# Performance work log

Hardware: AMD Instinct MI355X
Metric: run time of the kernel (lower is better)

## Reference

```python
import jax, jax.numpy as jnp
import numpy as np

N = 100000      # nodes
E = 1_600_000   # edges
IN = 128        # in_channels
HID = 32        # hidden_channels (per head)
HEADS = 4
NC = 10         # num_classes
NEG_SLOPE = 0.2 # GATConv leaky relu slope
BN_EPS = 1e-5


def _gat_conv(x, src, dst, W, a_src, a_dst, bias, heads, out_ch, concat):
    # x: [N, F_in]; W: [F_in, heads*out_ch]; a_src/a_dst: [heads, out_ch]
    n = x.shape[0]
    h = (x @ W).reshape(n, heads, out_ch)                    # [N,H,C]
    al_src = jnp.sum(h * a_src, axis=-1)                     # [N,H]
    al_dst = jnp.sum(h * a_dst, axis=-1)                     # [N,H]
    e = jax.nn.leaky_relu(al_src[src] + al_dst[dst], NEG_SLOPE)  # [E,H]
    # segment softmax over destination node
    m = jax.ops.segment_max(e, dst, num_segments=n)          # [N,H]
    ex = jnp.exp(e - m[dst])
    s = jax.ops.segment_sum(ex, dst, num_segments=n)         # [N,H]
    alpha = ex / (s[dst] + 1e-16)                            # [E,H]
    out = jax.ops.segment_sum(h[src] * alpha[:, :, None], dst, num_segments=n)  # [N,H,C]
    if concat:
        out = out.reshape(n, heads * out_ch)
    else:
        out = out.mean(axis=1)
    return out + bias


def _bn(x, gamma, beta, mean, var):
    # eval-mode BatchNorm1d with running stats
    return (x - mean) * jax.lax.rsqrt(var + BN_EPS) * gamma + beta


def setup_inputs() -> dict:
    key = jax.random.key(0)
    ks = iter(jax.random.split(key, 40))
    d = {}
    d['x'] = jax.random.normal(next(ks), (N, IN), dtype=jnp.float32)
    d['edge_index'] = jax.random.randint(next(ks), (2, E), 0, N, dtype=jnp.int32)
    dims = [(IN, HID, HEADS), (HID * HEADS, HID, HEADS), (HID * HEADS, HID, 1)]
    for i, (fin, c, h) in enumerate(dims):
        d[f'W{i}'] = jax.random.normal(next(ks), (fin, h * c), dtype=jnp.float32) * (1.0 / np.sqrt(fin))
        d[f'as{i}'] = jax.random.normal(next(ks), (h, c), dtype=jnp.float32) * 0.1
        d[f'ad{i}'] = jax.random.normal(next(ks), (h, c), dtype=jnp.float32) * 0.1
        bdim = h * c if i < 2 else c
        d[f'b{i}'] = jnp.zeros((bdim,), dtype=jnp.float32)
        d[f'g{i}'] = jax.random.uniform(next(ks), (bdim,), dtype=jnp.float32, minval=0.5, maxval=1.5)
        d[f'bt{i}'] = jax.random.normal(next(ks), (bdim,), dtype=jnp.float32) * 0.1
        d[f'm{i}'] = jax.random.normal(next(ks), (bdim,), dtype=jnp.float32) * 0.1
        d[f'v{i}'] = jax.random.uniform(next(ks), (bdim,), dtype=jnp.float32, minval=0.5, maxval=1.5)
    d['Wc'] = jax.random.normal(next(ks), (HID, NC), dtype=jnp.float32) * (1.0 / np.sqrt(HID))
    d['bc'] = jnp.zeros((NC,), dtype=jnp.float32)
    return d


def reference(x, edge_index, W0, as0, ad0, b0, g0, bt0, m0, v0,
              W1, as1, ad1, b1, g1, bt1, m1, v1,
              W2, as2, ad2, b2, g2, bt2, m2, v2, Wc, bc):
    src, dst = edge_index[0], edge_index[1]
    # layer 0: concat heads
    h = _gat_conv(x, src, dst, W0, as0, ad0, b0, HEADS, HID, True)
    h = jax.nn.elu(_bn(h, g0, bt0, m0, v0))
    # layer 1: concat heads
    h = _gat_conv(h, src, dst, W1, as1, ad1, b1, HEADS, HID, True)
    h = jax.nn.elu(_bn(h, g1, bt1, m1, v1))
    # layer 2: single head, no concat
    h = _gat_conv(h, src, dst, W2, as2, ad2, b2, 1, HID, False)
    h = jax.nn.elu(_bn(h, g2, bt2, m2, v2))
    # dropout is identity in eval mode
    return h @ Wc + bc
```

## Files before the change

kernel.cpp:

```cpp
#include <hip/hip_runtime.h>
#include <hip/hip_bf16.h>
#include <math.h>

#define NN   100000
#define NE   1600000
#define FIN  128
#define HID  32
#define NHEADS 4
#define NCLS 10

typedef unsigned int uint32;
typedef __fp16 half2_t __attribute__((ext_vector_type(2)));
typedef __fp16 half8_t __attribute__((ext_vector_type(8)));
typedef float  f32x4   __attribute__((ext_vector_type(4)));

__device__ __forceinline__ uint32 packh2(float a, float b) {
    half2_t h = __builtin_amdgcn_cvt_pkrtz(a, b);
    return __builtin_bit_cast(uint32, h);
}
__device__ __forceinline__ float h_lo(uint32 v) {
    return (float)__builtin_bit_cast(half2_t, v)[0];
}
__device__ __forceinline__ float h_hi(uint32 v) {
    return (float)__builtin_bit_cast(half2_t, v)[1];
}
__device__ __forceinline__ half8_t as_h8(uint4 v) {
    return __builtin_bit_cast(half8_t, v);
}

__global__ void zero_i32(int* __restrict__ p, int n) {
    int i = blockIdx.x * blockDim.x + threadIdx.x;
    if (i < n) p[i] = 0;
}

__global__ void hist_rank_kernel(const int* __restrict__ dst, int* __restrict__ cnt,
                                 int* __restrict__ rank, int e) {
    const int t0 = blockIdx.x * (blockDim.x * 4) + threadIdx.x;
    int d[4];
    bool a[4];
#pragma unroll
    for (int k = 0; k < 4; ++k) {
        const int j = t0 + k * 256;
        a[k] = (j < e);
        d[k] = a[k] ? dst[j] : 0;
    }
    int r[4];
#pragma unroll
    for (int k = 0; k < 4; ++k)
        if (a[k]) r[k] = atomicAdd(&cnt[d[k]], 1);
#pragma unroll
    for (int k = 0; k < 4; ++k) {
        const int j = t0 + k * 256;
        if (a[k]) rank[j] = r[k];
    }
}

__global__ void scan_block_sums(const int* __restrict__ cnt, int* __restrict__ bsum, int n) {
    __shared__ int sm[256];
    int i = blockIdx.x * 256 + threadIdx.x;
    int v = (i < n) ? cnt[i] : 0;
    sm[threadIdx.x] = v;
    __syncthreads();
    for (int off = 128; off > 0; off >>= 1) {
        if (threadIdx.x < off) sm[threadIdx.x] += sm[threadIdx.x + off];
        __syncthreads();
    }
    if (threadIdx.x == 0) bsum[blockIdx.x] = sm[0];
}

__global__ void scan_single(const int* __restrict__ bsum, int* __restrict__ boff, int nb) {
    __shared__ int sm[512];
    int t = threadIdx.x;
    int v = (t < nb) ? bsum[t] : 0;
    sm[t] = v;
    __syncthreads();
    for (int off = 1; off < 512; off <<= 1) {
        int u = (t >= off) ? sm[t - off] : 0;
        __syncthreads();
        sm[t] += u;
        __syncthreads();
    }
    if (t < nb) boff[t] = sm[t] - v;
}

__global__ void scan_final(const int* __restrict__ cnt, const int* __restrict__ boff,
                           int* __restrict__ rowptr, int n) {
    __shared__ int sm[256];
    int i = blockIdx.x * 256 + threadIdx.x;
    int v = (i < n) ? cnt[i] : 0;
    sm[threadIdx.x] = v;
    __syncthreads();
    for (int off = 1; off < 256; off <<= 1) {
        int u = (threadIdx.x >= off) ? sm[threadIdx.x - off] : 0;
        __syncthreads();
        sm[threadIdx.x] += u;
        __syncthreads();
    }
    int incl = sm[threadIdx.x];
    int excl = incl - v;
    if (i < n) rowptr[i] = boff[blockIdx.x] + excl;
    if (i == n - 1) rowptr[n] = boff[blockIdx.x] + incl;
}

__global__ void scatter_kernel(const int* __restrict__ src, const int* __restrict__ dst,
                               const int* __restrict__ rank, const int* __restrict__ rowptr,
                               int* __restrict__ esrc, int e) {
    const int t0 = blockIdx.x * (blockDim.x * 4) + threadIdx.x;
#pragma unroll
    for (int k = 0; k < 4; ++k) {
        const int j = t0 + k * 256;
        if (j < e) {
            const int d = dst[j];
            esrc[rowptr[d] + rank[j]] = src[j];
        }
    }
}

__global__ void conv_x_kernel(const float* __restrict__ x, uint32* __restrict__ Xh, int n4) {
    int i = blockIdx.x * blockDim.x + threadIdx.x;
    if (i >= n4) return;
    const float4 v = ((const float4*)x)[i];
    ((uint2*)Xh)[i] = make_uint2(packh2(v.x, v.y), packh2(v.z, v.w));
}

__global__ void conv_w_kernel(const float* __restrict__ W0, const float* __restrict__ W1,
                              const float* __restrict__ W2, uint32* __restrict__ Wt0,
                              uint32* __restrict__ Wt1, uint32* __restrict__ Wt2) {
    int t = blockIdx.x * blockDim.x + threadIdx.x;
    if (t < 8192) {
        const int nn = t >> 6, ku = t & 63;
        Wt0[t] = packh2(W0[(2 * ku) * 128 + nn], W0[(2 * ku + 1) * 128 + nn]);
    } else if (t < 16384) {
        const int l = t - 8192;
        const int nn = l >> 6, ku = l & 63;
        Wt1[l] = packh2(W1[(2 * ku) * 128 + nn], W1[(2 * ku + 1) * 128 + nn]);
    } else if (t < 18432) {
        const int l = t - 16384;
        const int nn = l >> 6, ku = l & 63;
        Wt2[l] = packh2(W2[(2 * ku) * 32 + nn], W2[(2 * ku + 1) * 32 + nn]);
    }
}

__global__ void bn_prep_kernel(
    const float* __restrict__ b0, const float* __restrict__ g0, const float* __restrict__ bt0,
    const float* __restrict__ m0, const float* __restrict__ v0,
    const float* __restrict__ b1, const float* __restrict__ g1, const float* __restrict__ bt1,
    const float* __restrict__ m1, const float* __restrict__ v1,
    const float* __restrict__ b2, const float* __restrict__ g2, const float* __restrict__ bt2,
    const float* __restrict__ m2, const float* __restrict__ v2,
    float* __restrict__ A, float* __restrict__ B) {
    const int t = threadIdx.x;
    const float *b, *g, *bt, *m, *v;
    int c;
    if (t < 128)      { b = b0; g = g0; bt = bt0; m = m0; v = v0; c = t; }
    else if (t < 256) { b = b1; g = g1; bt = bt1; m = m1; v = v1; c = t - 128; }
    else if (t < 288) { b = b2; g = g2; bt = bt2; m = m2; v = v2; c = t - 256; }
    else return;
    const float s = g[c] * rsqrtf(v[c] + 1e-5f);
    A[t] = s;
    B[t] = bt[c] + (b[c] - m[c]) * s;
}

template <int FOUT, int H>
__global__ __launch_bounds__(256) void gemm_mfma(const uint32* __restrict__ Xh,
                                                 const uint32* __restrict__ Wt,
                                                 const float* __restrict__ a_s,
                                                 const float* __restrict__ a_d,
                                                 float* __restrict__ alS,
                                                 float* __restrict__ alD,
                                                 uint32* __restrict__ Outh, int n) {
    constexpr int NT = FOUT / 16;
    const int wave = threadIdx.x >> 6;
    const int lane = threadIdx.x & 63;
    const int c = lane & 15;
    const int q = lane >> 4;
    const int row0 = blockIdx.x * 128 + wave * 32;

    int r0 = row0 + c;
    int r1 = row0 + 16 + c;
    if (r0 >= n) r0 = n - 1;
    if (r1 >= n) r1 = n - 1;

    f32x4 acc[2][NT];
#pragma unroll
    for (int m = 0; m < 2; ++m)
#pragma unroll
        for (int nt = 0; nt < NT; ++nt) acc[m][nt] = (f32x4){0.f, 0.f, 0.f, 0.f};

    const uint4* XU = (const uint4*)Xh;
    const uint4* WU = (const uint4*)Wt;

#pragma unroll
    for (int ks = 0; ks < 4; ++ks) {
        const half8_t a0 = as_h8(XU[(size_t)r0 * 16 + ks * 4 + q]);
        const half8_t a1 = as_h8(XU[(size_t)r1 * 16 + ks * 4 + q]);
#pragma unroll
        for (int nt = 0; nt < NT; ++nt) {
            const half8_t b = as_h8(WU[(nt * 16 + c) * 16 + ks * 4 + q]);
            acc[0][nt] = __builtin_amdgcn_mfma_f32_16x16x32_f16(a0, b, acc[0][nt], 0, 0, 0);
            acc[1][nt] = __builtin_amdgcn_mfma_f32_16x16x32_f16(a1, b, acc[1][nt], 0, 0, 0);
        }
    }

    float asv[NT], adv[NT];
#pragma unroll
    for (int nt = 0; nt < NT; ++nt) {
        asv[nt] = a_s[c + 16 * nt];
        adv[nt] = a_d[c + 16 * nt];
    }

#pragma unroll
    for (int m = 0; m < 2; ++m) {
#pragma unroll
        for (int reg = 0; reg < 4; ++reg) {
            const int grow = row0 + m * 16 + q * 4 + reg;
            const bool ok = (grow < n);
            if constexpr (H == 4) {
                float ps[4], pd[4];
#pragma unroll
                for (int h = 0; h < 4; ++h) {
                    ps[h] = acc[m][2 * h][reg] * asv[2 * h] + acc[m][2 * h + 1][reg] * asv[2 * h + 1];
                    pd[h] = acc[m][2 * h][reg] * adv[2 * h] + acc[m][2 * h + 1][reg] * adv[2 * h + 1];
                }
#pragma unroll
                for (int off = 1; off < 16; off <<= 1) {
#pragma unroll
                    for (int h = 0; h < 4; ++h) {
                        ps[h] += __shfl_xor(ps[h], off);
                        pd[h] += __shfl_xor(pd[h], off);
                    }
                }
                if (c < 4 && ok) {
                    const float vs = (c == 0) ? ps[0] : (c == 1) ? ps[1] : (c == 2) ? ps[2] : ps[3];
                    const float vd = (c == 0) ? pd[0] : (c == 1) ? pd[1] : (c == 2) ? pd[2] : pd[3];
                    alS[(size_t)grow * 4 + c] = vs;
                    alD[(size_t)grow * 4 + c] = vd;
                }
            } else {
                float ps = acc[m][0][reg] * asv[0] + acc[m][1][reg] * asv[1];
                float pd = acc[m][0][reg] * adv[0] + acc[m][1][reg] * adv[1];
#pragma unroll
                for (int off = 1; off < 16; off <<= 1) {
                    ps += __shfl_xor(ps, off);
                    pd += __shfl_xor(pd, off);
                }
                if (c == 0 && ok) {
                    alS[grow] = ps;
                    alD[grow] = pd;
                }
            }
#pragma unroll
            for (int nt = 0; nt < NT; ++nt) {
                const float v = acc[m][nt][reg];
                const float o = __shfl_xor(v, 1);
                if (((c & 1) == 0) && ok) {
                    Outh[(size_t)grow * (FOUT / 2) + nt * 8 + (c >> 1)] = packh2(v, o);
                }
            }
        }
    }
}

template <int H, int C>
__global__ __launch_bounds__(256) void gat_aggregate(
    const uint32* __restrict__ Hb,
    const int* __restrict__ rowptr, const int* __restrict__ esrc,
    const float* __restrict__ alS, const float* __restrict__ alD,
    const float* __restrict__ bnA, const float* __restrict__ bnB,
    uint32* __restrict__ B16, int n) {
    constexpr int F    = H * C;
    constexpr int RU4  = F / 8;
    constexpr int SLOTS = 64 / RU4;
    constexpr int UNROLL = 16 / SLOTS;

    const int wave = threadIdx.x >> 6;
    const int lane = threadIdx.x & 63;
    int d = blockIdx.x * 4 + wave;
    if (d >= n) return;
    d = __builtin_amdgcn_readfirstlane(d);

    const int li = lane & (RU4 - 1);
    const int g  = lane / RU4;
    const int head = (H == 4) ? (li >> 2) : 0;

    const float ald = alD[(size_t)d * H + head];
    const int beg = rowptr[d];
    const int end = rowptr[d + 1];
    const int endm1 = end - 1;

    float acc[8];
#pragma unroll
    for (int k = 0; k < 8; ++k) acc[k] = 0.f;
    float den = 0.f;

    const uint4* HbU4 = (const uint4*)Hb;

    for (int base = beg; base < end; base += 16) {
#pragma unroll
        for (int u = 0; u < UNROLL; ++u) {
            const int j  = base + u * SLOTS + g;
            const bool act = (j < end);
            const int jc = act ? j : endm1;
            const int sj = esrc[jc];
            const float aw = (H == 4) ? alS[(size_t)sj * 4 + head] : alS[sj];
            float t = aw + ald;
            t = fmaxf(t, 0.2f * t);
            const float ex = act ? __expf(t) : 0.f;
            den += ex;
            const uint4 v = HbU4[(size_t)sj * RU4 + li];
            acc[0] = fmaf(h_lo(v.x), ex, acc[0]);
            acc[1] = fmaf(h_hi(v.x), ex, acc[1]);
            acc[2] = fmaf(h_lo(v.y), ex, acc[2]);
            acc[3] = fmaf(h_hi(v.y), ex, acc[3]);
            acc[4] = fmaf(h_lo(v.z), ex, acc[4]);
            acc[5] = fmaf(h_hi(v.z), ex, acc[5]);
            acc[6] = fmaf(h_lo(v.w), ex, acc[6]);
            acc[7] = fmaf(h_hi(v.w), ex, acc[7]);
        }
    }

#pragma unroll
    for (int off = RU4; off < 64; off <<= 1) {
#pragma unroll
        for (int k = 0; k < 8; ++k) acc[k] += __shfl_xor(acc[k], off);
        den += __shfl_xor(den, off);
    }

    if (lane < RU4) {
        const float inv = 1.f / (den + 1e-16f);
        const int c0 = 8 * li;
        const float4 A0 = *(const float4*)(bnA + c0);
        const float4 A1 = *(const float4*)(bnA + c0 + 4);
        const float4 B0 = *(const float4*)(bnB + c0);
        const float4 B1 = *(const float4*)(bnB + c0 + 4);
        const float As[8] = {A0.x, A0.y, A0.z, A0.w, A1.x, A1.y, A1.z, A1.w};
        const float Bs[8] = {B0.x, B0.y, B0.z, B0.w, B1.x, B1.y, B1.z, B1.w};
        float y[8];
#pragma unroll
        for (int k = 0; k < 8; ++k) {
            const float yy = acc[k] * inv * As[k] + Bs[k];
            y[k] = yy > 0.f ? yy : expm1f(yy);
        }
        uint4 o;
        o.x = packh2(y[0], y[1]);
        o.y = packh2(y[2], y[3]);
        o.z = packh2(y[4], y[5]);
        o.w = packh2(y[6], y[7]);
        ((uint4*)B16)[(size_t)d * RU4 + li] = o;
    }
}

__global__ void classifier_kernel(const uint32* __restrict__ H3, const float* __restrict__ Wc,
                                  const float* __restrict__ bc, float* __restrict__ out, int n) {
    int t  = blockIdx.x * blockDim.x + threadIdx.x;
    int ni = t / NCLS, c = t % NCLS;
    if (ni >= n) return;
    const uint32* row = H3 + (size_t)ni * 16;
    float a = bc[c];
#pragma unroll
    for (int u = 0; u < 16; ++u) {
        const uint32 v = row[u];
        a = fmaf(h_lo(v), Wc[(2 * u) * NCLS + c], a);
        a = fmaf(h_hi(v), Wc[(2 * u + 1) * NCLS + c], a);
    }
    out[(size_t)ni * NCLS + c] = a;
}

static inline char* align256(char* p) {
    return (char*)(((uintptr_t)p + 255) & ~(uintptr_t)255);
}

extern "C" void kernel_launch(void* const* d_in, const int* in_sizes, int n_in,
                              void* d_out, int out_size, void* d_ws, size_t ws_size,
                              hipStream_t stream) {
    const float* x  = (const float*)d_in[0];
    const int*   ei = (const int*)d_in[1];
    const int N = in_sizes[0] / FIN;
    const int E = in_sizes[1] / 2;
    const int* src = ei;
    const int* dst = ei + E;

    const float *W0 = (const float*)d_in[2],  *as0 = (const float*)d_in[3],
                *ad0 = (const float*)d_in[4], *b0 = (const float*)d_in[5],
                *g0 = (const float*)d_in[6],  *bt0 = (const float*)d_in[7],
                *m0 = (const float*)d_in[8],  *v0 = (const float*)d_in[9];
    const float *W1 = (const float*)d_in[10], *as1 = (const float*)d_in[11],
                *ad1 = (const float*)d_in[12],*b1 = (const float*)d_in[13],
                *g1 = (const float*)d_in[14], *bt1 = (const float*)d_in[15],
                *m1 = (const float*)d_in[16], *v1 = (const float*)d_in[17];
    const float *W2 = (const float*)d_in[18], *as2 = (const float*)d_in[19],
                *ad2 = (const float*)d_in[20],*b2 = (const float*)d_in[21],
                *g2 = (const float*)d_in[22], *bt2 = (const float*)d_in[23],
                *m2 = (const float*)d_in[24], *v2 = (const float*)d_in[25];
    const float *Wc = (const float*)d_in[26], *bc = (const float*)d_in[27];
    float* out = (float*)d_out;

    char* p = (char*)d_ws;
    uint32* Xh  = (uint32*)p;   p = align256(p + (size_t)N * 64 * 4);
    uint32* Ht  = (uint32*)p;   p = align256(p + (size_t)N * 64 * 4);
    uint32* B16 = (uint32*)p;   p = align256(p + (size_t)N * 64 * 4);
    uint32* Wt0 = (uint32*)p;   p = align256(p + 8192 * 4);
    uint32* Wt1 = (uint32*)p;   p = align256(p + 8192 * 4);
    uint32* Wt2 = (uint32*)p;   p = align256(p + 2048 * 4);
    float* alS = (float*)p;     p = align256(p + (size_t)N * NHEADS * 4);
    float* alD = (float*)p;     p = align256(p + (size_t)N * NHEADS * 4);
    int* cnt = (int*)p;         p = align256(p + (size_t)N * 4);
    int* rowptr = (int*)p;      p = align256(p + (size_t)(N + 1) * 4);
    int* rank = (int*)p;        p = align256(p + (size_t)E * 4);
    int* esrc = (int*)p;        p = align256(p + (size_t)E * 4);
    int* bsum = (int*)p;        p = align256(p + 512 * 4);
    int* boff = (int*)p;        p = align256(p + 512 * 4);
    float* bnA = (float*)p;     p = align256(p + 288 * 4);
    float* bnB = (float*)p;     p = align256(p + 288 * 4);
    (void)ws_size; (void)n_in; (void)out_size;

    const int NB = (N + 255) / 256;
    const int EB4 = (E + 1023) / 1024;

    zero_i32<<<NB, 256, 0, stream>>>(cnt, N);
    hist_rank_kernel<<<EB4, 256, 0, stream>>>(dst, cnt, rank, E);
    scan_block_sums<<<NB, 256, 0, stream>>>(cnt, bsum, N);
    scan_single<<<1, 512, 0, stream>>>(bsum, boff, NB);
    scan_final<<<NB, 256, 0, stream>>>(cnt, boff, rowptr, N);
    scatter_kernel<<<EB4, 256, 0, stream>>>(src, dst, rank, rowptr, esrc, E);

    conv_x_kernel<<<(N * 32 + 255) / 256, 256, 0, stream>>>(x, Xh, N * 32);
    conv_w_kernel<<<72, 256, 0, stream>>>(W0, W1, W2, Wt0, Wt1, Wt2);
    bn_prep_kernel<<<1, 320, 0, stream>>>(b0, g0, bt0, m0, v0,
                                          b1, g1, bt1, m1, v1,
                                          b2, g2, bt2, m2, v2, bnA, bnB);

    const int GB = (N + 127) / 128;
    const int AB = (N + 3) / 4;

    gemm_mfma<128, 4><<<GB, 256, 0, stream>>>(Xh, Wt0, as0, ad0, alS, alD, Ht, N);
    gat_aggregate<4, 32><<<AB, 256, 0, stream>>>(Ht, rowptr, esrc, alS, alD,
                                                 bnA, bnB, B16, N);
    gemm_mfma<128, 4><<<GB, 256, 0, stream>>>(B16, Wt1, as1, ad1, alS, alD, Ht, N);
    gat_aggregate<4, 32><<<AB, 256, 0, stream>>>(Ht, rowptr, esrc, alS, alD,
                                                 bnA + 128, bnB + 128, B16, N);
    gemm_mfma<32, 1><<<GB, 256, 0, stream>>>(B16, Wt2, as2, ad2, alS, alD, Ht, N);
    gat_aggregate<1, 32><<<AB, 256, 0, stream>>>(Ht, rowptr, esrc, alS, alD,
                                                 bnA + 256, bnB + 256, B16, N);
    classifier_kernel<<<(N * NCLS + 255) / 256, 256, 0, stream>>>(B16, Wc, bc, out, N);
}
```

Baseline: 545.3 us.

## Fuse x conversion into first GEMM, add nontemporal hints, restructure classifier

Removes the separate fp32-to-fp16 conversion kernel for x by converting on the fly inside the first MFMA GEMM, which saves one full read and write pass over x. Adds nontemporal loads and stores in the CSR build, the edge-source gather and the aggregate output. Also rewrites the classifier so each thread computes all 10 classes for one node from vector loads. The trade-off is that the first GEMM now reads twice the bytes as fp32, and the nontemporal hints may hurt if those lines would otherwise be reused from cache.

```diff
diff --git a/kernel.cpp b/kernel.cpp
--- a/kernel.cpp
+++ b/kernel.cpp
@@ -13,6 +13,7 @@
 typedef __fp16 half2_t __attribute__((ext_vector_type(2)));
 typedef __fp16 half8_t __attribute__((ext_vector_type(8)));
 typedef float  f32x4   __attribute__((ext_vector_type(4)));
+typedef uint32 u32x4   __attribute__((ext_vector_type(4)));
 
 __device__ __forceinline__ uint32 packh2(float a, float b) {
     half2_t h = __builtin_amdgcn_cvt_pkrtz(a, b);
@@ -42,7 +43,7 @@
     for (int k = 0; k < 4; ++k) {
         const int j = t0 + k * 256;
         a[k] = (j < e);
-        d[k] = a[k] ? dst[j] : 0;
+        d[k] = a[k] ? __builtin_nontemporal_load(&dst[j]) : 0;
     }
     int r[4];
 #pragma unroll
@@ -51,7 +52,7 @@
 #pragma unroll
     for (int k = 0; k < 4; ++k) {
         const int j = t0 + k * 256;
-        if (a[k]) rank[j] = r[k];
+        if (a[k]) __builtin_nontemporal_store(r[k], &rank[j]);
     }
 }
 
@@ -110,17 +111,12 @@
     for (int k = 0; k < 4; ++k) {
         const int j = t0 + k * 256;
         if (j < e) {
-            const int d = dst[j];
-            esrc[rowptr[d] + rank[j]] = src[j];
-        }
-    }
-}
-
-__global__ void conv_x_kernel(const float* __restrict__ x, uint32* __restrict__ Xh, int n4) {
-    int i = blockIdx.x * blockDim.x + threadIdx.x;
-    if (i >= n4) return;
-    const float4 v = ((const float4*)x)[i];
-    ((uint2*)Xh)[i] = make_uint2(packh2(v.x, v.y), packh2(v.z, v.w));
+            const int d = __builtin_nontemporal_load(&dst[j]);
+            const int s = __builtin_nontemporal_load(&src[j]);
+            const int r = __builtin_nontemporal_load(&rank[j]);
+            __builtin_nontemporal_store(s, &esrc[rowptr[d] + r]);
+        }
+    }
 }
 
 __global__ void conv_w_kernel(const float* __restrict__ W0, const float* __restrict__ W1,
@@ -161,8 +157,8 @@
     B[t] = bt[c] + (b[c] - m[c]) * s;
 }
 
-template <int FOUT, int H>
-__global__ __launch_bounds__(256) void gemm_mfma(const uint32* __restrict__ Xh,
+template <int FOUT, int H, bool CONVA>
+__global__ __launch_bounds__(256) void gemm_mfma(const void* __restrict__ Xv,
                                                  const uint32* __restrict__ Wt,
                                                  const float* __restrict__ a_s,
                                                  const float* __restrict__ a_d,
@@ -187,13 +183,26 @@
 #pragma unroll
         for (int nt = 0; nt < NT; ++nt) acc[m][nt] = (f32x4){0.f, 0.f, 0.f, 0.f};
 
-    const uint4* XU = (const uint4*)Xh;
-    const uint4* WU = (const uint4*)Wt;
+    const uint4*  XU = (const uint4*)Xv;
+    const float4* XF = (const float4*)Xv;
+    const uint4*  WU = (const uint4*)Wt;
 
 #pragma unroll
     for (int ks = 0; ks < 4; ++ks) {
-        const half8_t a0 = as_h8(XU[(size_t)r0 * 16 + ks * 4 + q]);
-        const half8_t a1 = as_h8(XU[(size_t)r1 * 16 + ks * 4 + q]);
+        half8_t a0, a1;
+        if constexpr (CONVA) {
+            const float4 f0 = XF[(size_t)r0 * 32 + (ks * 4 + q) * 2];
+            const float4 f1 = XF[(size_t)r0 * 32 + (ks * 4 + q) * 2 + 1];
+            a0 = as_h8(make_uint4(packh2(f0.x, f0.y), packh2(f0.z, f0.w),
+                                  packh2(f1.x, f1.y), packh2(f1.z, f1.w)));
+            const float4 g0 = XF[(size_t)r1 * 32 + (ks * 4 + q) * 2];
+            const float4 g1 = XF[(size_t)r1 * 32 + (ks * 4 + q) * 2 + 1];
+            a1 = as_h8(make_uint4(packh2(g0.x, g0.y), packh2(g0.z, g0.w),
+                                  packh2(g1.x, g1.y), packh2(g1.z, g1.w)));
+        } else {
+            a0 = as_h8(XU[(size_t)r0 * 16 + ks * 4 + q]);
+            a1 = as_h8(XU[(size_t)r1 * 16 + ks * 4 + q]);
+        }
 #pragma unroll
         for (int nt = 0; nt < NT; ++nt) {
             const half8_t b = as_h8(WU[(nt * 16 + c) * 16 + ks * 4 + q]);
@@ -301,7 +310,7 @@
             const int j  = base + u * SLOTS + g;
             const bool act = (j < end);
             const int jc = act ? j : endm1;
-            const int sj = esrc[jc];
+            const int sj = __builtin_nontemporal_load(&esrc[jc]);
             const float aw = (H == 4) ? alS[(size_t)sj * 4 + head] : alS[sj];
             float t = aw + ald;
             t = fmaxf(t, 0.2f * t);
@@ -341,29 +350,43 @@
             const float yy = acc[k] * inv * As[k] + Bs[k];
             y[k] = yy > 0.f ? yy : expm1f(yy);
         }
-        uint4 o;
+        u32x4 o;
         o.x = packh2(y[0], y[1]);
         o.y = packh2(y[2], y[3]);
         o.z = packh2(y[4], y[5]);
         o.w = packh2(y[6], y[7]);
-        ((uint4*)B16)[(size_t)d * RU4 + li] = o;
-    }
-}
-
-__global__ void classifier_kernel(const uint32* __restrict__ H3, const float* __restrict__ Wc,
-                                  const float* __restrict__ bc, float* __restrict__ out, int n) {
-    int t  = blockIdx.x * blockDim.x + threadIdx.x;
-    int ni = t / NCLS, c = t % NCLS;
+        __builtin_nontemporal_store(o, (u32x4*)B16 + (size_t)d * RU4 + li);
+    }
+}
+
+__global__ __launch_bounds__(256) void classifier_kernel(
+    const uint32* __restrict__ H3, const float* __restrict__ Wc,
+    const float* __restrict__ bc, float* __restrict__ out, int n) {
+    const int ni = blockIdx.x * blockDim.x + threadIdx.x;
     if (ni >= n) return;
-    const uint32* row = H3 + (size_t)ni * 16;
-    float a = bc[c];
-#pragma unroll
-    for (int u = 0; u < 16; ++u) {
-        const uint32 v = row[u];
-        a = fmaf(h_lo(v), Wc[(2 * u) * NCLS + c], a);
-        a = fmaf(h_hi(v), Wc[(2 * u + 1) * NCLS + c], a);
-    }
-    out[(size_t)ni * NCLS + c] = a;
+    const uint4* row = (const uint4*)(H3 + (size_t)ni * 16);
+    float xf[32];
+#pragma unroll
+    for (int u = 0; u < 4; ++u) {
+        const uint4 v = row[u];
+        xf[u * 8 + 0] = h_lo(v.x); xf[u * 8 + 1] = h_hi(v.x);
+        xf[u * 8 + 2] = h_lo(v.y); xf[u * 8 + 3] = h_hi(v.y);
+        xf[u * 8 + 4] = h_lo(v.z); xf[u * 8 + 5] = h_hi(v.z);
+        xf[u * 8 + 6] = h_lo(v.w); xf[u * 8 + 7] = h_hi(v.w);
+    }
+    float o[NCLS];
+#pragma unroll
+    for (int c = 0; c < NCLS; ++c) o[c] = bc[c];
+#pragma unroll
+    for (int u = 0; u < 32; ++u) {
+#pragma unroll
+        for (int c = 0; c < NCLS; ++c) o[c] = fmaf(xf[u], Wc[u * NCLS + c], o[c]);
+    }
+    float* orow = out + (size_t)ni * NCLS;
+#pragma unroll
+    for (int c = 0; c < NCLS; c += 2) {
+        *(float2*)(orow + c) = make_float2(o[c], o[c + 1]);
+    }
 }
 
 static inline char* align256(char* p) {
@@ -396,7 +419,6 @@
     float* out = (float*)d_out;
 
     char* p = (char*)d_ws;
-    uint32* Xh  = (uint32*)p;   p = align256(p + (size_t)N * 64 * 4);
     uint32* Ht  = (uint32*)p;   p = align256(p + (size_t)N * 64 * 4);
     uint32* B16 = (uint32*)p;   p = align256(p + (size_t)N * 64 * 4);
     uint32* Wt0 = (uint32*)p;   p = align256(p + 8192 * 4);
@@ -424,7 +446,6 @@
     scan_final<<<NB, 256, 0, stream>>>(cnt, boff, rowptr, N);
     scatter_kernel<<<EB4, 256, 0, stream>>>(src, dst, rank, rowptr, esrc, E);
 
-    conv_x_kernel<<<(N * 32 + 255) / 256, 256, 0, stream>>>(x, Xh, N * 32);
     conv_w_kernel<<<72, 256, 0, stream>>>(W0, W1, W2, Wt0, Wt1, Wt2);
     bn_prep_kernel<<<1, 320, 0, stream>>>(b0, g0, bt0, m0, v0,
                                           b1, g1, bt1, m1, v1,
@@ -433,14 +454,14 @@
     const int GB = (N + 127) / 128;
     const int AB = (N + 3) / 4;
 
-    gemm_mfma<128, 4><<<GB, 256, 0, stream>>>(Xh, Wt0, as0, ad0, alS, alD, Ht, N);
+    gemm_mfma<128, 4, true><<<GB, 256, 0, stream>>>(x, Wt0, as0, ad0, alS, alD, Ht, N);
     gat_aggregate<4, 32><<<AB, 256, 0, stream>>>(Ht, rowptr, esrc, alS, alD,
                                                  bnA, bnB, B16, N);
-    gemm_mfma<128, 4><<<GB, 256, 0, stream>>>(B16, Wt1, as1, ad1, alS, alD, Ht, N);
+    gemm_mfma<128, 4, false><<<GB, 256, 0, stream>>>(B16, Wt1, as1, ad1, alS, alD, Ht, N);
     gat_aggregate<4, 32><<<AB, 256, 0, stream>>>(Ht, rowptr, esrc, alS, alD,
                                                  bnA + 128, bnB + 128, B16, N);
-    gemm_mfma<32, 1><<<GB, 256, 0, stream>>>(B16, Wt2, as2, ad2, alS, alD, Ht, N);
+    gemm_mfma<32, 1, false><<<GB, 256, 0, stream>>>(B16, Wt2, as2, ad2, alS, alD, Ht, N);
     gat_aggregate<1, 32><<<AB, 256, 0, stream>>>(Ht, rowptr, esrc, alS, alD,
                                                  bnA + 256, bnB + 256, B16, N);
-    classifier_kernel<<<(N * NCLS + 255) / 256, 256, 0, stream>>>(B16, Wc, bc, out, N);
-}
+    classifier_kernel<<<(N + 255) / 256, 256, 0, stream>>>(B16, Wc, bc, out, N);
+}
```

Result: slower. 557.9 us (+2.3%).
